# Performance work log

Measured on AMD Instinct MI355X. Metric: run time of the kernel, lower is better.

## Reference

```python
import jax, jax.numpy as jnp
import numpy as np

OBS_SIZE = 128
ACTION_SIZE = 10
B = 64
T = 512
FEAT = 512          # HIDDEN_SIZE
H = 256             # HIDDEN_MEMORY_SIZE


def setup_inputs() -> dict:
    key = jax.random.key(0)
    ks = jax.random.split(key, 16)
    s = 0.05
    return {
        "obs": jax.random.normal(ks[0], (B, T, OBS_SIZE), jnp.float32),
        "action": jax.random.randint(ks[1], (B * T,), 0, ACTION_SIZE, jnp.int64 if jax.config.jax_enable_x64 else jnp.int32),
        "masks": jax.random.randint(ks[2], (B, T - 1), 0, 2, jnp.int32),
        "old_hidden_memory": jax.random.normal(ks[3], (B, 1, H), jnp.float32),
        # fnn: Linear(obs_size, 512) + ReLU
        "W1": jax.random.normal(ks[4], (FEAT, OBS_SIZE), jnp.float32) * s,
        "b1": jnp.zeros((FEAT,), jnp.float32),
        # GRU weights, PyTorch layout: gates ordered (r, z, n)
        "W_ih": jax.random.normal(ks[5], (3 * H, FEAT), jnp.float32) * s,
        "W_hh": jax.random.normal(ks[6], (3 * H, H), jnp.float32) * s,
        "b_ih": jnp.zeros((3 * H,), jnp.float32),
        "b_hh": jnp.zeros((3 * H,), jnp.float32),
        # actor / critic heads
        "Wa": jax.random.normal(ks[7], (ACTION_SIZE, H), jnp.float32) * s,
        "ba": jnp.zeros((ACTION_SIZE,), jnp.float32),
        "Wc": jax.random.normal(ks[8], (1, H), jnp.float32) * s,
        "bc": jnp.zeros((1,), jnp.float32),
    }


def _evaluate_action(obs, old_hidden_memory, W1, b1, W_ih, W_hh, b_ih, b_hh,
                     Wa, ba, Wc, bc, action, masks):
    # feature extractor: Linear + ReLU  [B,T,FEAT]
    feat = jax.nn.relu(jnp.einsum('bto,fo->btf', obs, W1) + b1)

    # Precompute input-side gate projections once: [T,B,3H]
    gx = jnp.einsum('btf,gf->tbg', feat, W_ih) + b_ih

    # mask sequence: prepend a column of ones, per the torch code -> [T,B]
    mask_seq = jnp.concatenate(
        [jnp.ones((1, B), jnp.float32), masks.astype(jnp.float32).T], axis=0)

    h0 = old_hidden_memory[:, 0]  # [B,H]

    def cell(h, inp):
        gx_t, m_t = inp
        h = h * m_t[:, None]                       # episode-reset masking
        gh = h @ W_hh.T + b_hh                     # [B,3H]
        r = jax.nn.sigmoid(gx_t[:, :H] + gh[:, :H])
        z = jax.nn.sigmoid(gx_t[:, H:2 * H] + gh[:, H:2 * H])
        n = jnp.tanh(gx_t[:, 2 * H:] + r * gh[:, 2 * H:])
        h_new = (1.0 - z) * n + z * h
        return h_new, h_new

    _, hs = jax.lax.scan(cell, h0, (gx, mask_seq))  # hs: [T,B,H]
    hs = hs.transpose(1, 0, 2).reshape(B * T, H)    # flatten(end_dim=1)

    logits = hs @ Wa.T + ba                         # [BT,A]
    logp = jax.nn.log_softmax(logits, axis=-1)
    log_prob = jnp.take_along_axis(logp, action[:, None].astype(jnp.int32), axis=1)[:, 0]
    entropy = -jnp.sum(jnp.exp(logp) * logp, axis=-1)
    value = hs @ Wc.T + bc                          # [BT,1]
    return value, log_prob, entropy


def reference(obs, action, masks, old_hidden_memory, W1, b1, W_ih, W_hh,
              b_ih, b_hh, Wa, ba, Wc, bc):
    return _evaluate_action(obs, old_hidden_memory, W1, b1, W_ih, W_hh,
                            b_ih, b_hh, Wa, ba, Wc, bc, action, masks)
```

## Files before the change

kernel.cpp:

```cpp
#include <hip/hip_runtime.h>
#include <hip/hip_fp16.h>
#include <stdint.h>

#define B_    64
#define T_    512
#define OBS_  128
#define FEAT_ 512
#define H_    256
#define G_    768
#define BT_   32768
#define NSLOT 16

typedef _Float16 f16x8 __attribute__((ext_vector_type(8)));
typedef float    f32x4 __attribute__((ext_vector_type(4)));

__device__ __forceinline__ uint32_t h2u(__half2 h){ union{ __half2 h; uint32_t u; } c; c.h = h; return c.u; }
__device__ __forceinline__ __half2 u2h(uint32_t u){ union{ uint32_t u; __half2 h; } c; c.u = u; return c.h; }

__device__ __forceinline__ int sw(int r, int c) { return r * 128 + ((c ^ (r & 7)) << 4); }

__device__ __forceinline__ uint4 cvt8(float4 a, float4 b) {
    uint4 u;
    u.x = h2u(__floats2half2_rn(a.x, a.y));
    u.y = h2u(__floats2half2_rn(a.z, a.w));
    u.z = h2u(__floats2half2_rn(b.x, b.y));
    u.w = h2u(__floats2half2_rn(b.z, b.w));
    return u;
}

__global__ __launch_bounds__(512, 4)
void fused_gemm(const float* __restrict__ obs, const __half* __restrict__ W1h,
                const __half* __restrict__ Wihh, const float* __restrict__ b1,
                const float* __restrict__ bih, uint32_t* __restrict__ gxC)
{
    __shared__ __align__(16) __half smem[32768];
    __half* obsA  = smem;
    __half* featL = smem + 8192;
    __half* BsS   = smem + 16384;

    const int bid = blockIdx.x;
    const int m0 = (bid & 511) * 64;
    const int n0 = (bid >> 9) * 256;
    const int tid = threadIdx.x;
    const int lane = tid & 63, wn = tid >> 6;
    const int l15 = lane & 15, lq = lane >> 4;

    {
        const int r = tid >> 3, cpair = (tid & 7) * 2;
        #pragma unroll
        for (int c = 0; c < 2; ++c) {
            const int cc = cpair + c;
            const float* ap = obs + (size_t)(m0 + r) * OBS_ + cc * 8;
            const float4 f0 = ((const float4*)ap)[0];
            const float4 f1 = ((const float4*)ap)[1];
            *(uint4*)((char*)obsA + (cc >> 3) * 8192 + sw(r, cc & 7)) = cvt8(f0, f1);
        }
    }

    f32x4 acc2[4][2];
    #pragma unroll
    for (int i = 0; i < 4; ++i)
        #pragma unroll
        for (int jj = 0; jj < 2; ++jj) { const f32x4 z = {0.f,0.f,0.f,0.f}; acc2[i][jj] = z; }

    for (int j = 0; j < 4; ++j) {
        f32x4 acc1[4];
        #pragma unroll
        for (int i = 0; i < 4; ++i) { const f32x4 z = {0.f,0.f,0.f,0.f}; acc1[i] = z; }
        #pragma unroll
        for (int kt = 0; kt < 2; ++kt) {
            __syncthreads();
            if (tid < 256) {
                const int sr = tid >> 1, scb = (tid & 1) * 4;
                const __half* bp = W1h + (size_t)(j * 128 + sr) * OBS_ + kt * 64 + scb * 8;
                #pragma unroll
                for (int c = 0; c < 4; ++c)
                    *(uint4*)((char*)BsS + sw(sr, scb + c)) = ((const uint4*)bp)[c];
            }
            __syncthreads();
            #pragma unroll
            for (int kc = 0; kc < 2; ++kc) {
                f16x8 af[4];
                #pragma unroll
                for (int mi = 0; mi < 4; ++mi)
                    af[mi] = *(const f16x8*)((const char*)obsA + kt * 8192 +
                                             sw(mi * 16 + l15, kc * 4 + lq));
                const f16x8 bf = *(const f16x8*)((const char*)BsS +
                                                 sw(wn * 16 + l15, kc * 4 + lq));
                #pragma unroll
                for (int mi = 0; mi < 4; ++mi)
                    acc1[mi] = __builtin_amdgcn_mfma_f32_16x16x32_f16(af[mi], bf, acc1[mi], 0, 0, 0);
            }
        }
        {
            const int col = wn * 16 + l15;
            const float bv = b1[j * 128 + col];
            #pragma unroll
            for (int mi = 0; mi < 4; ++mi) {
                const f32x4 d = acc1[mi];
                #pragma unroll
                for (int rr = 0; rr < 4; ++rr) {
                    const float v = fmaxf(d[rr] + bv, 0.0f);
                    const uint32_t u = (uint32_t)__half_as_ushort(__float2half(v));
                    const uint32_t nb = (uint32_t)__shfl_xor((int)u, 1);
                    if (!(lane & 1)) {
                        const int row = mi * 16 + lq * 4 + rr;
                        *(uint32_t*)((char*)featL + (col >> 6) * 8192 + row * 128 +
                                     ((((col >> 3) & 7) ^ (row & 7)) << 4) + (col & 7) * 2) = u | (nb << 16);
                    }
                }
            }
        }
        #pragma unroll
        for (int kt2 = 0; kt2 < 2; ++kt2) {
            __syncthreads();
            {
                const int sr = tid >> 1, scb = (tid & 1) * 4;
                const __half* bp = Wihh + (size_t)(n0 + sr) * FEAT_ + j * 128 + kt2 * 64 + scb * 8;
                #pragma unroll
                for (int c = 0; c < 4; ++c)
                    *(uint4*)((char*)BsS + sw(sr, scb + c)) = ((const uint4*)bp)[c];
            }
            __syncthreads();
            #pragma unroll
            for (int kc = 0; kc < 2; ++kc) {
                f16x8 af[4], bf[2];
                #pragma unroll
                for (int mi = 0; mi < 4; ++mi)
                    af[mi] = *(const f16x8*)((const char*)featL + kt2 * 8192 +
                                             sw(mi * 16 + l15, kc * 4 + lq));
                #pragma unroll
                for (int ni = 0; ni < 2; ++ni)
                    bf[ni] = *(const f16x8*)((const char*)BsS +
                                             sw(wn * 32 + ni * 16 + l15, kc * 4 + lq));
                #pragma unroll
                for (int mi = 0; mi < 4; ++mi)
                    #pragma unroll
                    for (int ni = 0; ni < 2; ++ni)
                        acc2[mi][ni] = __builtin_amdgcn_mfma_f32_16x16x32_f16(af[mi], bf[ni], acc2[mi][ni], 0, 0, 0);
            }
        }
    }

    __syncthreads();
    uint32_t* Cs = (uint32_t*)smem;
    #pragma unroll
    for (int ni = 0; ni < 2; ++ni) {
        const int col = wn * 32 + ni * 16 + l15;
        const float bv = bih[n0 + col];
        #pragma unroll
        for (int mi = 0; mi < 4; ++mi) {
            const f32x4 d = acc2[mi][ni];
            #pragma unroll
            for (int rr = 0; rr < 4; ++rr) {
                const float v = d[rr] + bv;
                const uint32_t u = (uint32_t)__half_as_ushort(__float2half(v));
                const uint32_t nb = (uint32_t)__shfl_xor((int)u, 1);
                if (!(lane & 1))
                    Cs[(mi * 16 + lq * 4 + rr) * 128 + (col >> 1)] = u | (nb << 16);
            }
        }
    }
    __syncthreads();
    const int orow = tid >> 3, oseg = (tid & 7) * 16;
    #pragma unroll
    for (int c = 0; c < 4; ++c) {
        const uint4 val = *(const uint4*)&Cs[orow * 128 + oseg + c * 4];
        *(uint4*)(gxC + (size_t)(m0 + orow) * (G_ / 2) + (n0 >> 1) + oseg + c * 4) = val;
    }
}

__global__ void pack_half(const float* __restrict__ in, uint32_t* __restrict__ out, int n2)
{
    int i = blockIdx.x * 256 + threadIdx.x;
    if (i < n2) {
        float2 f = ((const float2*)in)[i];
        out[i] = h2u(__floats2half2_rn(f.x, f.y));
    }
}

__global__ void pack_whh(const float* __restrict__ Whh, uint32_t* __restrict__ outR,
                         uint32_t* __restrict__ outL, int* __restrict__ qctl)
{
    if (blockIdx.x == 0 && threadIdx.x == 0) { qctl[0] = 0; qctl[1] = 0; }
    int p = blockIdx.x * 256 + threadIdx.x;
    if (p >= 512 * 192) return;
    const int v4 = p >> 2, sub = p & 3;
    const int t = v4 / 48, ic = v4 - t * 48;
    const int i = ic >> 3, c = ic & 7;
    const int w = t >> 6, lane = t & 63;
    const int row = w * 96 + i * 16 + (lane & 15);
    const int kb = c * 32 + ((lane >> 4) << 3) + sub * 2;
    const uint32_t val = h2u(__floats2half2_rn(Whh[row * 256 + kb], Whh[row * 256 + kb + 1]));
    if (c < 6) outR[(t * 36 + i * 6 + c) * 4 + sub] = val;
    else       outL[(((i << 1) + (c - 6)) * 512 + t) * 4 + sub] = val;
}

__global__ __launch_bounds__(512)
void seg_build(const int* __restrict__ masks, int* __restrict__ queue,
               int* __restrict__ qtail)
{
    __shared__ int sc[512];
    __shared__ int starts[512];
    __shared__ int cshr[2];
    const int b = blockIdx.x, s = threadIdx.x;
    const int is = (s == 0) || (masks[b * (T_ - 1) + s - 1] == 0);
    sc[s] = is;
    __syncthreads();
    #pragma unroll
    for (int off = 1; off < 512; off <<= 1) {
        int v = (s >= off) ? sc[s - off] : 0;
        __syncthreads();
        sc[s] += v;
        __syncthreads();
    }
    if (is) starts[sc[s] - 1] = s;
    if (s == 511) cshr[0] = sc[511];
    __syncthreads();
    const int cnt = cshr[0];
    int valid = 0, st = 0, ln = 0;
    if (s < cnt) {
        st = starts[s];
        const int nxt = (s + 1 < cnt) ? starts[s + 1] : T_;
        ln = nxt - st;
        valid = (st == 0 || ln >= 2) ? 1 : 0;
    }
    sc[s] = valid;
    __syncthreads();
    #pragma unroll
    for (int off = 1; off < 512; off <<= 1) {
        int v = (s >= off) ? sc[s - off] : 0;
        __syncthreads();
        sc[s] += v;
        __syncthreads();
    }
    if (s == 511) cshr[1] = atomicAdd(qtail, sc[511]);
    __syncthreads();
    if (valid) queue[cshr[1] + sc[s] - 1] = (b << 19) | (st << 10) | ln;
}

__global__ __launch_bounds__(256)
void h0pre(const __half* __restrict__ gx, const float* __restrict__ bhh,
           const int* __restrict__ masks, uint32_t* __restrict__ hs2)
{
    for (int row = blockIdx.x; row < B_ * (T_ - 1); row += gridDim.x) {
        if (masks[row] != 0) continue;
        const int b = row / (T_ - 1), t = 1 + row - b * (T_ - 1);
        const int e = threadIdx.x;
        const __half* grow = gx + (size_t)(b * T_ + t) * 768;
        const float gxr = __half2float(grow[e]);
        const float gxz = __half2float(grow[e + 256]);
        const float gxn = __half2float(grow[e + 512]);
        const float rg = 1.f / (1.f + exp2f(-(gxr + bhh[e]) * 1.44269504f));
        const float zg = 1.f / (1.f + exp2f(-(gxz + bhh[e + 256]) * 1.44269504f));
        const float nin = gxn + rg * bhh[e + 512];
        const float e2x = exp2f(nin * 2.885390082f);
        const float ng = 1.f - 2.f / (e2x + 1.f);
        const float hnew = (1.f - zg) * ng;
        const float other = __shfl_xor(hnew, 1);
        if (!(e & 1)) hs2[(size_t)(b * T_ + t) * 128 + (e >> 1)] = h2u(__floats2half2_rn(hnew, other));
    }
}

__global__ __launch_bounds__(512, 2)
void gru_mfma(const __half* __restrict__ gx, const uint4* __restrict__ WhhR,
              const uint4* __restrict__ WhhL, const float* __restrict__ bhh,
              const float* __restrict__ h0, const int* __restrict__ queue,
              const int* __restrict__ qctl, uint32_t* __restrict__ hs2)
{
    __shared__ __align__(16) __half Hl[NSLOT * 256];
    __shared__ __align__(16) __half Plh[NSLOT * 784];
    __shared__ __align__(16) uint4  Wl[12 * 512];
    __shared__ float Bl[G_];
    __shared__ int s_end[NSLOT], s_row[NSLOT], s_act[NSLOT], s_nxt[NSLOT];
    __shared__ int cur;

    const int tid = threadIdx.x;
    const int lane = tid & 63, w = tid >> 6;
    const int s = tid >> 5, g32 = tid & 31, e0 = g32 * 8;
    const int col = lane & 15, lq = lane >> 4;

    f16x8 wr[36];
    {
        const f16x8* wp = (const f16x8*)(WhhR + (size_t)tid * 36);
        #pragma unroll
        for (int i = 0; i < 36; ++i) wr[i] = wp[i];
    }
    #pragma unroll
    for (int i = 0; i < 12; ++i) Wl[i * 512 + tid] = WhhL[i * 512 + tid];
    if (tid < 384) { Bl[tid] = bhh[tid]; Bl[tid + 384] = bhh[tid + 384]; }
    { const uint4 z4 = {0u, 0u, 0u, 0u}; *(uint4*)((char*)Hl + tid * 16) = z4; }

    const int NQ = qctl[0];
    const int gb = blockIdx.x;
    const int lo = (int)(((long long)NQ * gb) >> 8);
    const int hi = (int)(((long long)NQ * (gb + 1)) >> 8);
    if (tid == 0) cur = lo + NSLOT;
    __syncthreads();

    {
        int e = -1;
        if (lo + s < hi) e = queue[lo + s];
        if (e >= 0) {
            const int ln = e & 1023, st = (e >> 10) & 511, nb = e >> 19;
            uint4 hseed;
            if (st == 0) {
                const float4 a = *(const float4*)(h0 + nb * 256 + e0);
                const float4 b = *(const float4*)(h0 + nb * 256 + e0 + 4);
                hseed = cvt8(a, b);
                if (g32 == 0) { s_row[s] = nb * T_; s_end[s] = nb * T_ + ln; }
            } else {
                hseed = *(const uint4*)(hs2 + (size_t)(nb * T_ + st) * 128 + g32 * 4);
                if (g32 == 0) { s_row[s] = nb * T_ + st + 1; s_end[s] = nb * T_ + st + ln; }
            }
            *(uint4*)((char*)Hl + s * 512 + ((g32 ^ (s & 7)) << 4)) = hseed;
            if (g32 == 0) {
                s_act[s] = 1;
                const int p = atomicAdd(&cur, 1);
                s_nxt[s] = (p < hi) ? queue[p] : -1;
            }
        } else if (g32 == 0) {
            s_act[s] = 0; s_nxt[s] = -1; s_row[s] = 0; s_end[s] = 0;
        }
    }
    __syncthreads();

    for (;;) {
        bool alive = false;
        #pragma unroll
        for (int i = 0; i < NSLOT; ++i) alive |= (s_act[i] != 0);
        if (!alive) break;

        const int myrow = s_row[s];
        const int nxte = s_nxt[s];
        const __half* grow = gx + (size_t)myrow * G_;
        const f16x8 gr = *(const f16x8*)(grow + e0);
        const f16x8 gz = *(const f16x8*)(grow + 256 + e0);
        const f16x8 gn = *(const f16x8*)(grow + 512 + e0);
        uint4 su = {0u, 0u, 0u, 0u};
        if (nxte >= 0) {
            const int st = (nxte >> 10) & 511, nb = nxte >> 19;
            if (st == 0) {
                const float4 a = *(const float4*)(h0 + nb * 256 + e0);
                const float4 b = *(const float4*)(h0 + nb * 256 + e0 + 4);
                su = cvt8(a, b);
            } else {
                su = *(const uint4*)(hs2 + (size_t)(nb * T_ + st) * 128 + g32 * 4);
            }
        }
        f16x8 bfv[8];
        #pragma unroll
        for (int c = 0; c < 8; ++c)
            bfv[c] = *(const f16x8*)((const char*)Hl + col * 512 +
                                     ((((c << 2) + lq) ^ (col & 7)) << 4));
        f32x4 acc[6];
        #pragma unroll
        for (int i = 0; i < 6; ++i) { const f32x4 z = {0.f, 0.f, 0.f, 0.f}; acc[i] = z; }
        #pragma unroll
        for (int c = 0; c < 6; ++c)
            #pragma unroll
            for (int i = 0; i < 6; ++i)
                acc[i] = __builtin_amdgcn_mfma_f32_16x16x32_f16(wr[i * 6 + c], bfv[c], acc[i], 0, 0, 0);
        #pragma unroll
        for (int c2 = 0; c2 < 2; ++c2)
            #pragma unroll
            for (int i = 0; i < 6; ++i) {
                const f16x8 wlt = *(const f16x8*)&Wl[(i * 2 + c2) * 512 + tid];
                acc[i] = __builtin_amdgcn_mfma_f32_16x16x32_f16(wlt, bfv[6 + c2], acc[i], 0, 0, 0);
            }
        #pragma unroll
        for (int i = 0; i < 6; ++i) {
            uint2 ph;
            ph.x = h2u(__floats2half2_rn(acc[i][0], acc[i][1]));
            ph.y = h2u(__floats2half2_rn(acc[i][2], acc[i][3]));
            *(uint2*)(Plh + col * 784 + (w * 96 + i * 16 + lq * 4)) = ph;
        }
        asm volatile("s_waitcnt lgkmcnt(0)" ::: "memory");
        __builtin_amdgcn_s_barrier();

        if (s_act[s]) {
            const __half* Pr = Plh + s * 784;
            const f16x8 R  = *(const f16x8*)(Pr + e0);
            const f16x8 Z  = *(const f16x8*)(Pr + 256 + e0);
            const f16x8 Nn = *(const f16x8*)(Pr + 512 + e0);
            const f32x4 br0 = *(const f32x4*)(Bl + e0),       br1 = *(const f32x4*)(Bl + e0 + 4);
            const f32x4 bz0 = *(const f32x4*)(Bl + 256 + e0), bz1 = *(const f32x4*)(Bl + 256 + e0 + 4);
            const f32x4 bn0 = *(const f32x4*)(Bl + 512 + e0), bn1 = *(const f32x4*)(Bl + 512 + e0 + 4);
            const uint4 hp4 = *(const uint4*)((const char*)Hl + s * 512 + ((g32 ^ (s & 7)) << 4));
            const __half2 q0 = u2h(hp4.x), q1 = u2h(hp4.y), q2 = u2h(hp4.z), q3 = u2h(hp4.w);
            const float hpv[8] = { __low2float(q0), __high2float(q0), __low2float(q1), __high2float(q1),
                                   __low2float(q2), __high2float(q2), __low2float(q3), __high2float(q3) };
            float hn[8];
            #pragma unroll
            for (int j = 0; j < 8; ++j) {
                const float ghr = (float)R[j]  + (j < 4 ? br0[j] : br1[j - 4]);
                const float ghz = (float)Z[j]  + (j < 4 ? bz0[j] : bz1[j - 4]);
                const float ghn = (float)Nn[j] + (j < 4 ? bn0[j] : bn1[j - 4]);
                const float rg = 1.f / (1.f + exp2f(-((float)gr[j] + ghr) * 1.44269504f));
                const float zg = 1.f / (1.f + exp2f(-((float)gz[j] + ghz) * 1.44269504f));
                const float nin = (float)gn[j] + rg * ghn;
                const float ex = exp2f(nin * 2.885390082f);
                const float ng = 1.f - 2.f / (ex + 1.f);
                hn[j] = (1.f - zg) * ng + zg * hpv[j];
            }
            uint4 hp;
            hp.x = h2u(__floats2half2_rn(hn[0], hn[1]));
            hp.y = h2u(__floats2half2_rn(hn[2], hn[3]));
            hp.z = h2u(__floats2half2_rn(hn[4], hn[5]));
            hp.w = h2u(__floats2half2_rn(hn[6], hn[7]));
            *(uint4*)(hs2 + (size_t)myrow * 128 + g32 * 4) = hp;
            if (myrow + 1 < s_end[s]) {
                *(uint4*)((char*)Hl + s * 512 + ((g32 ^ (s & 7)) << 4)) = hp;
                if (g32 == 0) s_row[s] = myrow + 1;
            } else if (nxte >= 0) {
                const int ln = nxte & 1023, st = (nxte >> 10) & 511, nb = nxte >> 19;
                *(uint4*)((char*)Hl + s * 512 + ((g32 ^ (s & 7)) << 4)) = su;
                if (g32 == 0) {
                    if (st == 0) { s_row[s] = nb * T_;          s_end[s] = nb * T_ + ln; }
                    else         { s_row[s] = nb * T_ + st + 1; s_end[s] = nb * T_ + st + ln; }
                    const int p = atomicAdd(&cur, 1);
                    s_nxt[s] = (p < hi) ? queue[p] : -1;
                }
            } else if (g32 == 0) {
                s_act[s] = 0;
            }
        }
        asm volatile("s_waitcnt lgkmcnt(0)" ::: "memory");
        __builtin_amdgcn_s_barrier();
    }
}

__global__ __launch_bounds__(256)
void heads_kernel(const uint32_t* __restrict__ hs2, const float* __restrict__ Wa,
                  const float* __restrict__ ba, const float* __restrict__ Wc,
                  const float* __restrict__ bc, const int* __restrict__ action,
                  float* __restrict__ out)
{
    const int wid = threadIdx.x >> 6, lane = threadIdx.x & 63;
    const int row = blockIdx.x * 4 + wid;
    const uint2 hv2 = ((const uint2*)(hs2 + (size_t)row * 128))[lane];
    const __half2 ha = u2h(hv2.x), hb = u2h(hv2.y);
    const float h0f = __low2float(ha), h1f = __high2float(ha);
    const float h2f = __low2float(hb), h3f = __high2float(hb);
    float sums[11];
    #pragma unroll
    for (int n = 0; n < 11; ++n) {
        const float* wrow = (n < 10) ? (Wa + n * 256) : Wc;
        const float4 wv = ((const float4*)wrow)[lane];
        sums[n] = h0f * wv.x + h1f * wv.y + h2f * wv.z + h3f * wv.w;
    }
    #pragma unroll
    for (int n = 0; n < 11; ++n) {
        float v = sums[n];
        #pragma unroll
        for (int off = 32; off; off >>= 1) v += __shfl_xor(v, off);
        sums[n] = v;
    }
    float logits[10];
    #pragma unroll
    for (int n = 0; n < 10; ++n) logits[n] = sums[n] + ba[n];
    const float value = sums[10] + bc[0];
    float mx = logits[0];
    #pragma unroll
    for (int n = 1; n < 10; ++n) mx = fmaxf(mx, logits[n]);
    float ssum = 0.f, sdot = 0.f;
    #pragma unroll
    for (int n = 0; n < 10; ++n) {
        float d = logits[n] - mx;
        float e = exp2f(d * 1.44269504f);
        ssum += e; sdot += e * d;
    }
    const float lns = logf(ssum);
    const float lse = mx + lns;
    const float entropy = lns - sdot / ssum;
    const int a = action[row];
    float la = 0.f;
    #pragma unroll
    for (int n = 0; n < 10; ++n) la = (n == a) ? logits[n] : la;
    if (lane == 0) {
        out[row] = value;
        out[BT_ + row] = la - lse;
        out[2 * BT_ + row] = entropy;
    }
}

extern "C" void kernel_launch(void* const* d_in, const int* in_sizes, int n_in,
                              void* d_out, int out_size, void* d_ws, size_t ws_size,
                              hipStream_t stream)
{
    const float* obs    = (const float*)d_in[0];
    const int*   action = (const int*)d_in[1];
    const int*   masks  = (const int*)d_in[2];
    const float* h0     = (const float*)d_in[3];
    const float* W1     = (const float*)d_in[4];
    const float* b1     = (const float*)d_in[5];
    const float* Wih    = (const float*)d_in[6];
    const float* Whh    = (const float*)d_in[7];
    const float* bih    = (const float*)d_in[8];
    const float* bhh    = (const float*)d_in[9];
    const float* Wa     = (const float*)d_in[10];
    const float* ba     = (const float*)d_in[11];
    const float* Wc     = (const float*)d_in[12];
    const float* bc     = (const float*)d_in[13];
    float* out = (float*)d_out;

    char* p = (char*)d_ws;
    __half*   gx   = (__half*)p;    p += (size_t)BT_ * G_ * 2;
    uint32_t* hs2  = (uint32_t*)p;  p += (size_t)BT_ * H_ * 2;
    uint32_t* W1h  = (uint32_t*)p;  p += FEAT_ * OBS_ * 2;
    uint32_t* Wihh = (uint32_t*)p;  p += G_ * FEAT_ * 2;
    uint4*    WhhR = (uint4*)p;     p += 512 * 36 * 16;
    uint4*    WhhL = (uint4*)p;     p += 12 * 512 * 16;
    int*      queue= (int*)p;       p += B_ * 512 * 4;
    int*      qctl = (int*)p;       p += 256;

    pack_half<<<(FEAT_ * OBS_ / 2 + 255) / 256, 256, 0, stream>>>(W1, W1h, FEAT_ * OBS_ / 2);
    pack_half<<<(G_ * FEAT_ / 2 + 255) / 256, 256, 0, stream>>>(Wih, Wihh, G_ * FEAT_ / 2);
    pack_whh<<<384, 256, 0, stream>>>(Whh, (uint32_t*)WhhR, (uint32_t*)WhhL, qctl);
    seg_build<<<B_, 512, 0, stream>>>(masks, queue, &qctl[0]);
    fused_gemm<<<1536, 512, 0, stream>>>(obs, (const __half*)W1h, (const __half*)Wihh, b1, bih, (uint32_t*)gx);
    h0pre<<<2048, 256, 0, stream>>>(gx, bhh, masks, hs2);
    gru_mfma<<<256, 512, 0, stream>>>(gx, WhhR, WhhL, bhh, h0, queue, qctl, hs2);
    heads_kernel<<<8192, 256, 0, stream>>>(hs2, Wa, ba, Wc, bc, action, out);
}
```

Before: 203.7 us.

## Prepack GEMM weights into MFMA fragment layout and load B-operands directly to registers

Replaces the plain fp16 weight packing with a pack kernel that stores W1 and W_ih already arranged in MFMA B-fragment order per lane. The fused GEMM then loads B fragments straight from global memory into registers instead of staging them through shared memory. This removes the LDS B buffer, halves shared memory per block, and drops several syncthreads per K step. The cost is more global/L2 traffic per wave (each wave fetches its own fragments) and more live registers for the prefetched fragments.

```diff
diff --git a/kernel.cpp b/kernel.cpp
--- a/kernel.cpp
+++ b/kernel.cpp
@@ -29,18 +29,17 @@
 }
 
 __global__ __launch_bounds__(512, 4)
-void fused_gemm(const float* __restrict__ obs, const __half* __restrict__ W1h,
-                const __half* __restrict__ Wihh, const float* __restrict__ b1,
+void fused_gemm(const float* __restrict__ obs, const uint4* __restrict__ W1f,
+                const uint4* __restrict__ Wihf, const float* __restrict__ b1,
                 const float* __restrict__ bih, uint32_t* __restrict__ gxC)
 {
-    __shared__ __align__(16) __half smem[32768];
+    __shared__ __align__(16) __half smem[16384];
     __half* obsA  = smem;
     __half* featL = smem + 8192;
-    __half* BsS   = smem + 16384;
 
     const int bid = blockIdx.x;
     const int m0 = (bid & 511) * 64;
-    const int n0 = (bid >> 9) * 256;
+    const int nt = bid >> 9;
     const int tid = threadIdx.x;
     const int lane = tid & 63, wn = tid >> 6;
     const int l15 = lane & 15, lq = lane >> 4;
@@ -56,6 +55,7 @@
             *(uint4*)((char*)obsA + (cc >> 3) * 8192 + sw(r, cc & 7)) = cvt8(f0, f1);
         }
     }
+    __syncthreads();
 
     f32x4 acc2[4][2];
     #pragma unroll
@@ -64,20 +64,24 @@
         for (int jj = 0; jj < 2; ++jj) { const f32x4 z = {0.f,0.f,0.f,0.f}; acc2[i][jj] = z; }
 
     for (int j = 0; j < 4; ++j) {
+        uint4 w1f[4];
+        {
+            const uint4* base = W1f + ((size_t)(j * 8 + wn) * 4) * 64 + lane;
+            #pragma unroll
+            for (int q = 0; q < 4; ++q) w1f[q] = base[q * 64];
+        }
+        uint4 wif0[4];
+        #pragma unroll
+        for (int ni = 0; ni < 2; ++ni) {
+            const uint4* base = Wihf + ((size_t)(nt * 16 + wn * 2 + ni) * 16 + j * 4) * 64 + lane;
+            #pragma unroll
+            for (int kc = 0; kc < 2; ++kc) wif0[ni * 2 + kc] = base[kc * 64];
+        }
         f32x4 acc1[4];
         #pragma unroll
         for (int i = 0; i < 4; ++i) { const f32x4 z = {0.f,0.f,0.f,0.f}; acc1[i] = z; }
         #pragma unroll
-        for (int kt = 0; kt < 2; ++kt) {
-            __syncthreads();
-            if (tid < 256) {
-                const int sr = tid >> 1, scb = (tid & 1) * 4;
-                const __half* bp = W1h + (size_t)(j * 128 + sr) * OBS_ + kt * 64 + scb * 8;
-                #pragma unroll
-                for (int c = 0; c < 4; ++c)
-                    *(uint4*)((char*)BsS + sw(sr, scb + c)) = ((const uint4*)bp)[c];
-            }
-            __syncthreads();
+        for (int kt = 0; kt < 2; ++kt)
             #pragma unroll
             for (int kc = 0; kc < 2; ++kc) {
                 f16x8 af[4];
@@ -85,13 +89,11 @@
                 for (int mi = 0; mi < 4; ++mi)
                     af[mi] = *(const f16x8*)((const char*)obsA + kt * 8192 +
                                              sw(mi * 16 + l15, kc * 4 + lq));
-                const f16x8 bf = *(const f16x8*)((const char*)BsS +
-                                                 sw(wn * 16 + l15, kc * 4 + lq));
+                const f16x8 bf = *(const f16x8*)&w1f[kt * 2 + kc];
                 #pragma unroll
                 for (int mi = 0; mi < 4; ++mi)
                     acc1[mi] = __builtin_amdgcn_mfma_f32_16x16x32_f16(af[mi], bf, acc1[mi], 0, 0, 0);
             }
-        }
         {
             const int col = wn * 16 + l15;
             const float bv = b1[j * 128 + col];
@@ -111,43 +113,52 @@
                 }
             }
         }
-        #pragma unroll
-        for (int kt2 = 0; kt2 < 2; ++kt2) {
-            __syncthreads();
-            {
-                const int sr = tid >> 1, scb = (tid & 1) * 4;
-                const __half* bp = Wihh + (size_t)(n0 + sr) * FEAT_ + j * 128 + kt2 * 64 + scb * 8;
-                #pragma unroll
-                for (int c = 0; c < 4; ++c)
-                    *(uint4*)((char*)BsS + sw(sr, scb + c)) = ((const uint4*)bp)[c];
-            }
-            __syncthreads();
-            #pragma unroll
-            for (int kc = 0; kc < 2; ++kc) {
-                f16x8 af[4], bf[2];
+        __syncthreads();
+        uint4 wif1[4];
+        #pragma unroll
+        for (int ni = 0; ni < 2; ++ni) {
+            const uint4* base = Wihf + ((size_t)(nt * 16 + wn * 2 + ni) * 16 + j * 4 + 2) * 64 + lane;
+            #pragma unroll
+            for (int kc = 0; kc < 2; ++kc) wif1[ni * 2 + kc] = base[kc * 64];
+        }
+        #pragma unroll
+        for (int kc = 0; kc < 2; ++kc) {
+            f16x8 af[4];
+            #pragma unroll
+            for (int mi = 0; mi < 4; ++mi)
+                af[mi] = *(const f16x8*)((const char*)featL +
+                                         sw(mi * 16 + l15, kc * 4 + lq));
+            #pragma unroll
+            for (int ni = 0; ni < 2; ++ni) {
+                const f16x8 bf = *(const f16x8*)&wif0[ni * 2 + kc];
                 #pragma unroll
                 for (int mi = 0; mi < 4; ++mi)
-                    af[mi] = *(const f16x8*)((const char*)featL + kt2 * 8192 +
-                                             sw(mi * 16 + l15, kc * 4 + lq));
-                #pragma unroll
-                for (int ni = 0; ni < 2; ++ni)
-                    bf[ni] = *(const f16x8*)((const char*)BsS +
-                                             sw(wn * 32 + ni * 16 + l15, kc * 4 + lq));
+                    acc2[mi][ni] = __builtin_amdgcn_mfma_f32_16x16x32_f16(af[mi], bf, acc2[mi][ni], 0, 0, 0);
+            }
+        }
+        #pragma unroll
+        for (int kc = 0; kc < 2; ++kc) {
+            f16x8 af[4];
+            #pragma unroll
+            for (int mi = 0; mi < 4; ++mi)
+                af[mi] = *(const f16x8*)((const char*)featL + 8192 +
+                                         sw(mi * 16 + l15, kc * 4 + lq));
+            #pragma unroll
+            for (int ni = 0; ni < 2; ++ni) {
+                const f16x8 bf = *(const f16x8*)&wif1[ni * 2 + kc];
                 #pragma unroll
                 for (int mi = 0; mi < 4; ++mi)
-                    #pragma unroll
-                    for (int ni = 0; ni < 2; ++ni)
-                        acc2[mi][ni] = __builtin_amdgcn_mfma_f32_16x16x32_f16(af[mi], bf[ni], acc2[mi][ni], 0, 0, 0);
-            }
-        }
-    }
-
-    __syncthreads();
+                    acc2[mi][ni] = __builtin_amdgcn_mfma_f32_16x16x32_f16(af[mi], bf, acc2[mi][ni], 0, 0, 0);
+            }
+        }
+        __syncthreads();
+    }
+
     uint32_t* Cs = (uint32_t*)smem;
     #pragma unroll
     for (int ni = 0; ni < 2; ++ni) {
         const int col = wn * 32 + ni * 16 + l15;
-        const float bv = bih[n0 + col];
+        const float bv = bih[nt * 256 + col];
         #pragma unroll
         for (int mi = 0; mi < 4; ++mi) {
             const f32x4 d = acc2[mi][ni];
@@ -166,17 +177,23 @@
     #pragma unroll
     for (int c = 0; c < 4; ++c) {
         const uint4 val = *(const uint4*)&Cs[orow * 128 + oseg + c * 4];
-        *(uint4*)(gxC + (size_t)(m0 + orow) * (G_ / 2) + (n0 >> 1) + oseg + c * 4) = val;
-    }
-}
-
-__global__ void pack_half(const float* __restrict__ in, uint32_t* __restrict__ out, int n2)
-{
-    int i = blockIdx.x * 256 + threadIdx.x;
-    if (i < n2) {
-        float2 f = ((const float2*)in)[i];
-        out[i] = h2u(__floats2half2_rn(f.x, f.y));
-    }
+        *(uint4*)(gxC + (size_t)(m0 + orow) * (G_ / 2) + (nt * 128) + oseg + c * 4) = val;
+    }
+}
+
+template<int K>
+__global__ void pack_bfrag(const float* __restrict__ W, uint32_t* __restrict__ out, int total)
+{
+    int p = blockIdx.x * 256 + threadIdx.x;
+    if (p >= total) return;
+    const int e2 = p & 3;
+    const int l  = (p >> 2) & 63;
+    const int f  = p >> 8;
+    const int k32 = f & (K / 32 - 1);
+    const int ct  = f / (K / 32);
+    const int row = ct * 16 + (l & 15);
+    const int k   = k32 * 32 + ((l >> 4) << 3) + e2 * 2;
+    out[p] = h2u(__floats2half2_rn(W[(size_t)row * K + k], W[(size_t)row * K + k + 1]));
 }
 
 __global__ void pack_whh(const float* __restrict__ Whh, uint32_t* __restrict__ outR,
@@ -507,18 +524,18 @@
     char* p = (char*)d_ws;
     __half*   gx   = (__half*)p;    p += (size_t)BT_ * G_ * 2;
     uint32_t* hs2  = (uint32_t*)p;  p += (size_t)BT_ * H_ * 2;
-    uint32_t* W1h  = (uint32_t*)p;  p += FEAT_ * OBS_ * 2;
-    uint32_t* Wihh = (uint32_t*)p;  p += G_ * FEAT_ * 2;
+    uint32_t* W1f  = (uint32_t*)p;  p += FEAT_ * OBS_ * 2;
+    uint32_t* Wihf = (uint32_t*)p;  p += G_ * FEAT_ * 2;
     uint4*    WhhR = (uint4*)p;     p += 512 * 36 * 16;
     uint4*    WhhL = (uint4*)p;     p += 12 * 512 * 16;
     int*      queue= (int*)p;       p += B_ * 512 * 4;
     int*      qctl = (int*)p;       p += 256;
 
-    pack_half<<<(FEAT_ * OBS_ / 2 + 255) / 256, 256, 0, stream>>>(W1, W1h, FEAT_ * OBS_ / 2);
-    pack_half<<<(G_ * FEAT_ / 2 + 255) / 256, 256, 0, stream>>>(Wih, Wihh, G_ * FEAT_ / 2);
+    pack_bfrag<OBS_><<<128, 256, 0, stream>>>(W1, W1f, FEAT_ * OBS_ / 2);
+    pack_bfrag<FEAT_><<<768, 256, 0, stream>>>(Wih, Wihf, G_ * FEAT_ / 2);
     pack_whh<<<384, 256, 0, stream>>>(Whh, (uint32_t*)WhhR, (uint32_t*)WhhL, qctl);
     seg_build<<<B_, 512, 0, stream>>>(masks, queue, &qctl[0]);
-    fused_gemm<<<1536, 512, 0, stream>>>(obs, (const __half*)W1h, (const __half*)Wihh, b1, bih, (uint32_t*)gx);
+    fused_gemm<<<1536, 512, 0, stream>>>(obs, (const uint4*)W1f, (const uint4*)Wihf, b1, bih, (uint32_t*)gx);
     h0pre<<<2048, 256, 0, stream>>>(gx, bhh, masks, hs2);
     gru_mfma<<<256, 512, 0, stream>>>(gx, WhhR, WhhL, bhh, h0, queue, qctl, hs2);
     heads_kernel<<<8192, 256, 0, stream>>>(hs2, Wa, ba, Wc, bc, action, out);
```

After: 177.5 us. 12.9% less time.
